# Kernel optimization log

Measured on AMD Instinct MI355X. Metric: run time of the kernel, lower is better.

Reference implementation:

```python
import jax, jax.numpy as jnp
import numpy as np
import math

# ---- hyperparameters taken verbatim from the source losses ----
NSAMPLE_REP = 20      # ballquery nsample in get_repulsion_loss
RADIUS_REP = 0.07     # ballquery radius in get_repulsion_loss
H_REP = 0.03          # kernel bandwidth h
PERCENTAGES = (0.004, 0.008, 0.01, 0.012, 0.016)
UNI_RADIUS = 1.0


def _gather(p, idx):
    # p: [B, N, 3], idx: [B, ...] int -> [B, ..., 3]  (pointops.grouping/gathering)
    return jax.vmap(lambda pts, i: pts[i])(p, idx)


def _ballquery(radius, nsample, q, p):
    # pointops.ballquery: for each query, first `nsample` point indices within
    # radius, padded with the first found index. q:[B,M,3], p:[B,N,3] -> [B,M,nsample]
    d = jnp.sum((q[:, :, None, :] - p[:, None, :, :]) ** 2, -1)  # [B,M,N]
    N = p.shape[1]
    keys = jnp.where(d <= radius * radius,
                     jnp.arange(N, dtype=jnp.int32)[None, None, :], N)
    idx = jnp.sort(keys, axis=-1)[..., :nsample]
    return jnp.where(idx >= N, idx[..., :1], idx)  # pad misses with first hit


def _fps(pcd, npoint):
    # pointops.furthestsampling on [B,N,3] -> [B,npoint] int32
    B, N, _ = pcd.shape
    bidx = jnp.arange(B)

    def step(carry, _):
        dist, far = carry                         # [B,N], [B]
        pt = pcd[bidx, far]                       # [B,3]
        d = jnp.sum((pcd - pt[:, None, :]) ** 2, -1)
        dist = jnp.minimum(dist, d)
        nxt = jnp.argmax(dist, -1).astype(jnp.int32)
        return (dist, nxt), far

    init = (jnp.full((B, N), 1e10, pcd.dtype), jnp.zeros((B,), jnp.int32))
    _, idxs = jax.lax.scan(step, init, None, length=npoint)
    return idxs.T  # [B, npoint]


def _repulsion_loss(pred):
    # pred: [B, N, 3]
    idx = _ballquery(RADIUS_REP, NSAMPLE_REP, pred, pred)   # [B,N,20], detached ints
    g = _gather(pred, idx) - pred[:, :, None, :]            # [B,N,20,3]
    dists = jnp.sum(g * g, -1)                              # [B,N,20]
    vals, _ = jax.lax.top_k(-dists, 5)                      # 5 smallest sq-dists
    d5 = jnp.maximum(-vals[:, :, 1:], 0.0)                  # drop self, ReLU
    ds = jnp.sqrt(d5)
    w = jnp.exp(-d5 / (H_REP * H_REP))
    return jnp.mean(RADIUS_REP - ds * w)


def _uniform_loss(pcd):
    # pcd: [B, N, 3]
    N = pcd.shape[1]
    npoint = int(N * 0.05)
    # FPS is called with identical args for every percentage -> compute once.
    fps_idx = _fps(jax.lax.stop_gradient(pcd), npoint)
    new_xyz = _gather(pcd, fps_idx)                          # [B,npoint,3]
    loss = jnp.zeros((), pcd.dtype)
    for p in PERCENTAGES:
        nsample = int(N * p)
        r = math.sqrt(p * UNI_RADIUS)
        disk_area = math.pi * UNI_RADIUS ** 2 * p / nsample
        expect_len = math.sqrt(2 * disk_area / 1.732)
        idx = _ballquery(r, nsample, new_xyz, pcd)           # [B,npoint,nsample]
        grouped = _gather(pcd, idx).reshape(-1, nsample, 3)  # [B*npoint,nsample,3]
        # knn_point(2, grouped, grouped): pairwise sq-dists inside each disk
        d = jnp.sum((grouped[:, :, None, :] - grouped[:, None, :, :]) ** 2, -1)
        vals, _ = jax.lax.top_k(-d, 2)
        ud = -vals[:, :, 1:]                                  # nearest non-self sqdist
        ud = jnp.sqrt(jnp.abs(ud + 1e-8))
        ud = jnp.mean(ud, -1)
        ud = (ud - expect_len) ** 2 / (expect_len + 1e-8)
        loss = loss + jnp.mean(ud) * (p * 100.0) ** 2
    return loss / len(PERCENTAGES)


def setup_inputs() -> dict:
    key = jax.random.key(0)
    # refined upsampled cloud: B=4, r*N = 4*2048 = 8192 points in [-1,1]^3
    pcd = jax.random.uniform(key, (4, 8192, 3), jnp.float32) * 2.0 - 1.0
    return {"pcd": pcd}


def reference(pcd):
    return jnp.stack([_uniform_loss(pcd), _repulsion_loss(pcd)])
```

## Files before the change

### kernel.cpp

```cpp
#include <hip/hip_runtime.h>
#include <hip/hip_bf16.h>
#include <cmath>
#include <cfloat>

#define BATCH 4
#define NPTS 8192
#define NPOINT 409
#define NBALLS (BATCH * NPOINT)
#define REP_NS 20
#define REP_QB 64
#define REP_SEG 8
#define SEG_LEN (NPTS / REP_SEG)
#define REP_BLOCKS (BATCH * NPTS / REP_QB)

#define WCAP 160
#define HCAP (4 * WCAP)

#define WS_FPS_OFF 0
#define WS_REP_OFF 8192
#define WS_UNI_OFF 12288

typedef float v2f __attribute__((ext_vector_type(2)));

struct UniParams {
  float  thr[5];
  float  e[5];
  float  eden[5];
  int    ns[5];
};

template <int CTRL>
__device__ __forceinline__ unsigned long long dpp_max_u64(unsigned long long key) {
  const int lo = __builtin_amdgcn_update_dpp(
      0, (int)(unsigned)(key & 0xFFFFFFFFull), CTRL, 0xf, 0xf, true);
  const int hi = __builtin_amdgcn_update_dpp(
      0, (int)(unsigned)(key >> 32), CTRL, 0xf, 0xf, true);
  const unsigned long long ok =
      ((unsigned long long)(unsigned)hi << 32) | (unsigned)lo;
  return ok > key ? ok : key;
}

__device__ __forceinline__ void ins5(float v, float& t0, float& t1, float& t2,
                                     float& t3, float& t4) {
  if (v < t4) {
    t4 = v;
    if (t4 < t3) { float tmp = t3; t3 = t4; t4 = tmp; }
    if (t3 < t2) { float tmp = t2; t2 = t3; t3 = tmp; }
    if (t2 < t1) { float tmp = t1; t1 = t2; t2 = tmp; }
    if (t1 < t0) { float tmp = t0; t0 = t1; t1 = tmp; }
  }
}

__device__ __forceinline__ float rep_term(float d) {
  d = fmaxf(d, 0.0f);
  return 0.07f - sqrtf(d) * expf(-(d / 0.0009f));
}

__global__ __launch_bounds__(512, 2) void fpsrep_kernel(const float* __restrict__ pcd,
                                                        int* __restrict__ fps_idx,
                                                        double* __restrict__ rep_part,
                                                        float rep_thr) {
  const int tid = threadIdx.x;
  const int lane = tid & 63;
  const int w = tid >> 6;
  extern __shared__ float smem[];

  if (blockIdx.x < BATCH) {
    const int b = blockIdx.x;
    const float* P = pcd + b * NPTS * 3;
    float* X = smem;
    float* Y = smem + NPTS;
    float* Z = smem + 2 * NPTS;

    for (int i = tid; i < NPTS; i += 512) {
      X[i] = P[i * 3 + 0];
      Y[i] = P[i * 3 + 1];
      Z[i] = P[i * 3 + 2];
    }

    v2f px[8], py[8], pz[8], dist[8];
    const int base = tid * 16;
#pragma unroll
    for (int k = 0; k < 8; k++) {
      const int i0 = (base + 2 * k) * 3;
      const int i1 = (base + 2 * k + 1) * 3;
      px[k] = (v2f){P[i0 + 0], P[i1 + 0]};
      py[k] = (v2f){P[i0 + 1], P[i1 + 1]};
      pz[k] = (v2f){P[i0 + 2], P[i1 + 2]};
      dist[k] = (v2f){1e10f, 1e10f};
    }
#pragma unroll
    for (int k = 0; k < 8; k++) {
      asm volatile("" : "+v"(px[k]), "+v"(py[k]), "+v"(pz[k]));
    }

    __shared__ unsigned long long s_key[2][8];
    __syncthreads();

    int far = 0;
    float fx = X[0], fy = Y[0], fz = Z[0];
    for (int s = 0; s < NPOINT; s++) {
      if (tid == 0) fps_idx[b * NPOINT + s] = far;

      const v2f fxv = (v2f){fx, fx};
      const v2f fyv = (v2f){fy, fy};
      const v2f fzv = (v2f){fz, fz};
      float best = -1.0f;
      int kb = 0;
#pragma unroll
      for (int k = 0; k < 8; k++) {
#pragma clang fp contract(off)
        const v2f dx = px[k] - fxv;
        const v2f dy = py[k] - fyv;
        const v2f dz = pz[k] - fzv;
        const v2f d  = (dx * dx + dy * dy) + dz * dz;
        const float n0 = fminf(dist[k].x, d.x);
        const float n1 = fminf(dist[k].y, d.y);
        dist[k].x = n0;
        dist[k].y = n1;
        if (n0 > best) { best = n0; kb = 2 * k; }
        if (n1 > best) { best = n1; kb = 2 * k + 1; }
      }
      const int bidx = base + kb;
      unsigned long long key =
          ((unsigned long long)__float_as_uint(best) << 32) |
          (unsigned long long)(0xFFFFFFFFu - (unsigned)bidx);

      key = dpp_max_u64<0x111>(key);
      key = dpp_max_u64<0x112>(key);
      key = dpp_max_u64<0x114>(key);
      key = dpp_max_u64<0x118>(key);
      key = dpp_max_u64<0x142>(key);
      key = dpp_max_u64<0x143>(key);

      const int par = s & 1;
      if (lane == 63) s_key[par][w] = key;
      __syncthreads();
      unsigned long long kbk = s_key[par][0];
#pragma unroll
      for (int w2 = 1; w2 < 8; w2++) {
        const unsigned long long kk = s_key[par][w2];
        if (kk > kbk) kbk = kk;
      }
      far = (int)(0xFFFFFFFFu - (unsigned)(kbk & 0xFFFFFFFFull));
      fx = X[far];
      fy = Y[far];
      fz = Z[far];
    }
    return;
  }

  __shared__ float s_t5[REP_SEG][REP_QB][5];
  __shared__ float s_d0[REP_SEG][REP_QB];
  __shared__ int   s_cnt[REP_SEG][REP_QB];

  const int blk = blockIdx.x - BATCH;
  const int b = blk >> 7;
  const int q = ((blk & 127) << 6) + lane;
  const float* P = pcd + b * NPTS * 3;

  const float qx = P[q * 3 + 0], qy = P[q * 3 + 1], qz = P[q * 3 + 2];

  int cnt = 0;
  float d0 = 0.0f;
  float t0 = FLT_MAX, t1 = FLT_MAX, t2 = FLT_MAX, t3 = FLT_MAX, t4 = FLT_MAX;

  const int wu = __builtin_amdgcn_readfirstlane(w);
  const float* S = P + wu * SEG_LEN * 3;
#pragma unroll 4
  for (int i = 0; i < SEG_LEN; i++) {
    const float x = S[i * 3 + 0];
    const float y = S[i * 3 + 1];
    const float z = S[i * 3 + 2];
    const float dx = qx - x, dy = qy - y, dz = qz - z;
    const float d = dx * dx + dy * dy + dz * dz;
    if (d <= rep_thr && cnt < REP_NS) {
      if (cnt == 0) d0 = d;
      ins5(d, t0, t1, t2, t3, t4);
      cnt++;
    }
  }

  s_t5[w][lane][0] = t0; s_t5[w][lane][1] = t1; s_t5[w][lane][2] = t2;
  s_t5[w][lane][3] = t3; s_t5[w][lane][4] = t4;
  s_d0[w][lane] = d0;
  s_cnt[w][lane] = cnt;
  __syncthreads();

  if (w == 0) {
    int total = 0;
    float fd0 = 0.0f;
    int first_seen = 0;
    float m0 = FLT_MAX, m1 = FLT_MAX, m2 = FLT_MAX, m3 = FLT_MAX, m4 = FLT_MAX;
#pragma unroll
    for (int sg = 0; sg < REP_SEG; sg++) {
      const int c = s_cnt[sg][lane];
      if (c > 0 && !first_seen) { fd0 = s_d0[sg][lane]; first_seen = 1; }
      total += c;
#pragma unroll
      for (int j = 0; j < 5; j++) ins5(s_t5[sg][lane][j], m0, m1, m2, m3, m4);
    }

    if (total > REP_NS) {
      int c2 = 0;
      m0 = FLT_MAX; m1 = FLT_MAX; m2 = FLT_MAX; m3 = FLT_MAX; m4 = FLT_MAX;
      for (int i = 0; i < NPTS && c2 < REP_NS; i++) {
        const float dx = qx - P[i * 3 + 0];
        const float dy = qy - P[i * 3 + 1];
        const float dz = qz - P[i * 3 + 2];
        const float d = dx * dx + dy * dy + dz * dz;
        if (d <= rep_thr) { ins5(d, m0, m1, m2, m3, m4); c2++; }
      }
    } else {
      for (int c = total; c < REP_NS; c++) ins5(fd0, m0, m1, m2, m3, m4);
    }

    float sum = rep_term(m1) + rep_term(m2) + rep_term(m3) + rep_term(m4);
#pragma unroll
    for (int off = 32; off >= 1; off >>= 1) sum += __shfl_down(sum, off);
    if (lane == 0) rep_part[blk] = (double)sum;
  }
}

__global__ __launch_bounds__(256) void uni_kernel(const float* __restrict__ pcd,
                                                  const int* __restrict__ fps_idx,
                                                  double* __restrict__ uni_part,
                                                  UniParams up) {
  const int ball = blockIdx.x;
  const int b = ball / NPOINT;
  const int tid = threadIdx.x;
  const int lane = tid & 63, w = tid >> 6;
  const float* P = pcd + b * NPTS * 3;

  const int qidx = fps_idx[ball];
  const float qx = P[qidx * 3 + 0], qy = P[qidx * 3 + 1], qz = P[qidx * 3 + 2];

  __shared__ float wx[4][WCAP], wy[4][WCAP], wz[4][WCAP], wd[4][WCAP];
  __shared__ int   s_wcnt[4];
  __shared__ float FX[HCAP], FY[HCAP], FZ[HCAP], FD[HCAP];
  __shared__ float CX[5][131], CY[5][131], CZ[5][131];
  __shared__ double dpart[4];

  int wcnt = 0;
  const float* S = P + w * 2048 * 3;
  for (int it = 0; it < 32; it++) {
    const int j = it * 64 + lane;
    const float x = S[j * 3 + 0];
    const float y = S[j * 3 + 1];
    const float z = S[j * 3 + 2];
    const float dx = qx - x, dy = qy - y, dz = qz - z;
    const float d = dx * dx + dy * dy + dz * dz;
    const bool hit = (d <= up.thr[4]);
    const unsigned long long m = __ballot(hit);
    if (hit) {
      const int pos = wcnt + __popcll(m & ((1ull << lane) - 1ull));
      if (pos < WCAP) {
        wx[w][pos] = x; wy[w][pos] = y; wz[w][pos] = z; wd[w][pos] = d;
      }
    }
    wcnt += __popcll(m);
  }
  if (lane == 0) s_wcnt[w] = min(wcnt, WCAP);
  __syncthreads();

  int off = 0;
#pragma unroll
  for (int w2 = 0; w2 < 4; w2++) {
    if (w2 == w) break;
    off += s_wcnt[w2];
  }
  for (int i = lane; i < s_wcnt[w]; i += 64) {
    FX[off + i] = wx[w][i]; FY[off + i] = wy[w][i];
    FZ[off + i] = wz[w][i]; FD[off + i] = wd[w][i];
  }
  __syncthreads();
  const int c = s_wcnt[0] + s_wcnt[1] + s_wcnt[2] + s_wcnt[3];

  const double wj_tab[5] = {0.16 / (5.0 * 1636.0 * 32.0),
                            0.64 / (5.0 * 1636.0 * 65.0),
                            1.0  / (5.0 * 1636.0 * 81.0),
                            1.44 / (5.0 * 1636.0 * 98.0),
                            2.56 / (5.0 * 1636.0 * 131.0)};

  double local = 0.0;
  for (int jp = w; jp < 5; jp += ((w == 0) ? 4 : 8)) {
    const float thr = up.thr[jp];
    const int nsj = up.ns[jp];

    int cnt2 = 0;
    for (int bse = 0; bse < c; bse += 64) {
      const int e = bse + lane;
      const bool pred = (e < c) && (FD[e] <= thr);
      const unsigned long long m = __ballot(pred);
      if (pred) {
        const int pos = cnt2 + __popcll(m & ((1ull << lane) - 1ull));
        if (pos < nsj) {
          CX[jp][pos] = FX[e]; CY[jp][pos] = FY[e]; CZ[jp][pos] = FZ[e];
        }
      }
      cnt2 += __popcll(m);
    }
    const int cj = min(cnt2, nsj);
    const int pads = nsj - cj;
    const int istart = (pads > 0) ? 1 : 0;

    if (pads > 0 && lane == 0) {
      const float ud = sqrtf(fabsf(1e-8f));
      const float dd = ud - up.e[jp];
      const float tt = (dd * dd) / up.eden[jp];
      local += (double)tt * wj_tab[jp] * (double)(pads + 1);
    }

    for (int r = istart + lane; r < cj; r += 64) {
      const float xi = CX[jp][r], yi = CY[jp][r], zi = CZ[jp][r];
      float m2 = FLT_MAX;
      for (int e2 = 0; e2 < cj; e2++) {
        if (e2 == r) continue;
        const float dx = xi - CX[jp][e2];
        const float dy = yi - CY[jp][e2];
        const float dz = zi - CZ[jp][e2];
        const float d = dx * dx + dy * dy + dz * dz;
        if (d < m2) m2 = d;
      }
      const float ud = sqrtf(fabsf(m2 + 1e-8f));
      const float dd = ud - up.e[jp];
      const float tt = (dd * dd) / up.eden[jp];
      local += (double)tt * wj_tab[jp];
    }
  }

#pragma unroll
  for (int o = 32; o >= 1; o >>= 1) local += __shfl_down(local, o);
  if (lane == 0) dpart[w] = local;
  __syncthreads();
  if (tid == 0) {
    uni_part[ball] = dpart[0] + dpart[1] + dpart[2] + dpart[3];
  }
}

__global__ __launch_bounds__(256) void fin_kernel(const double* __restrict__ rep_part,
                                                  const double* __restrict__ uni_part,
                                                  float* __restrict__ out) {
  __shared__ double sd[256];
  const int t = threadIdx.x;
  double u = 0.0, r = 0.0;
  for (int i = t; i < NBALLS; i += 256) u += uni_part[i];
  for (int i = t; i < REP_BLOCKS; i += 256) r += rep_part[i];

  sd[t] = u; __syncthreads();
  for (int s = 128; s > 0; s >>= 1) { if (t < s) sd[t] += sd[t + s]; __syncthreads(); }
  const double usum = sd[0];
  __syncthreads();
  sd[t] = r; __syncthreads();
  for (int s = 128; s > 0; s >>= 1) { if (t < s) sd[t] += sd[t + s]; __syncthreads(); }

  if (t == 0) {
    out[0] = (float)usum;
    out[1] = (float)(sd[0] * (1.0 / 131072.0));
  }
}

extern "C" void kernel_launch(void* const* d_in, const int* in_sizes, int n_in,
                              void* d_out, int out_size, void* d_ws, size_t ws_size,
                              hipStream_t stream) {
  (void)in_sizes; (void)n_in; (void)out_size; (void)ws_size;
  const float* pcd = (const float*)d_in[0];
  float* out = (float*)d_out;
  int*    fps      = (int*)((char*)d_ws + WS_FPS_OFF);
  double* rep_part = (double*)((char*)d_ws + WS_REP_OFF);
  double* uni_part = (double*)((char*)d_ws + WS_UNI_OFF);

  const float rep_thr = (float)(0.07 * 0.07);

  UniParams up;
  const double ps[5] = {0.004, 0.008, 0.01, 0.012, 0.016};
  for (int j = 0; j < 5; j++) {
    const int ns = (int)(8192.0 * ps[j]);
    const double r = sqrt(ps[j]);
    up.thr[j] = (float)(r * r);
    const double disk = M_PI * ps[j] / (double)ns;
    const double el = sqrt(2.0 * disk / 1.732);
    up.e[j] = (float)el;
    up.eden[j] = (float)(el + 1e-8);
    up.ns[j] = ns;
  }

  static const int kDynLds = NPTS * 3 * (int)sizeof(float);
  (void)hipFuncSetAttribute((const void*)fpsrep_kernel,
                            hipFuncAttributeMaxDynamicSharedMemorySize, kDynLds);

  fpsrep_kernel<<<BATCH + REP_BLOCKS, 512, kDynLds, stream>>>(pcd, fps, rep_part,
                                                              rep_thr);
  uni_kernel<<<NBALLS, 256, 0, stream>>>(pcd, fps, uni_part, up);
  fin_kernel<<<1, 256, 0, stream>>>(rep_part, uni_part, out);
}
```

Measured before the change: 447.1 us.

## Fuse FPS, repulsion and uniform loss into persistent kernel with spin-wait overlap

Merges the repulsion and uniform-loss work into one persistent kernel alongside the FPS blocks. Worker blocks fetch tasks from an atomic counter, and uniform-loss tasks spin on FPS indices that are published with atomic stores. The goal is to hide the uniform-loss pass behind the serial FPS chain instead of running it after a kernel boundary. The cost is spin-waiting, large LDS per worker block that caps residency, and 512-thread blocks with 8 warps for the uni tasks, where 3 warps idle in the per-percentage stage.

```diff
diff --git a/kernel.cpp b/kernel.cpp
--- a/kernel.cpp
+++ b/kernel.cpp
@@ -8,17 +8,19 @@
 #define NPOINT 409
 #define NBALLS (BATCH * NPOINT)
 #define REP_NS 20
-#define REP_QB 64
 #define REP_SEG 8
 #define SEG_LEN (NPTS / REP_SEG)
-#define REP_BLOCKS (BATCH * NPTS / REP_QB)
-
-#define WCAP 160
-#define HCAP (4 * WCAP)
+#define REP_TASKS 512
+#define NTASKS (REP_TASKS + NBALLS)
+#define NWORKERS 252
+
+#define UW 96
+#define UH (8 * UW)
 
 #define WS_FPS_OFF 0
 #define WS_REP_OFF 8192
 #define WS_UNI_OFF 12288
+#define WS_CNT_OFF 25600
 
 typedef float v2f __attribute__((ext_vector_type(2)));
 
@@ -56,14 +58,27 @@
   return 0.07f - sqrtf(d) * expf(-(d / 0.0009f));
 }
 
-__global__ __launch_bounds__(512, 2) void fpsrep_kernel(const float* __restrict__ pcd,
-                                                        int* __restrict__ fps_idx,
-                                                        double* __restrict__ rep_part,
-                                                        float rep_thr) {
+__global__ __launch_bounds__(512, 2) void fused_kernel(const float* __restrict__ pcd,
+                                                       int* __restrict__ fps_idx,
+                                                       double* __restrict__ rep_part,
+                                                       double* __restrict__ uni_part,
+                                                       int* __restrict__ counter,
+                                                       UniParams up, float rep_thr) {
   const int tid = threadIdx.x;
   const int lane = tid & 63;
   const int w = tid >> 6;
   extern __shared__ float smem[];
+
+  __shared__ unsigned long long s_key[2][8];
+  __shared__ float s_t5[REP_SEG][64][5];
+  __shared__ float s_d0[REP_SEG][64];
+  __shared__ int   s_cnt[REP_SEG][64];
+  __shared__ float wx[8][UW], wy[8][UW], wz[8][UW], wd[8][UW];
+  __shared__ int   s_wcnt[8];
+  __shared__ float FX[UH], FY[UH], FZ[UH], FD[UH];
+  __shared__ float CX[5][131], CY[5][131], CZ[5][131];
+  __shared__ double dpart[8];
+  __shared__ int s_task, s_qidx;
 
   if (blockIdx.x < BATCH) {
     const int b = blockIdx.x;
@@ -94,13 +109,15 @@
       asm volatile("" : "+v"(px[k]), "+v"(py[k]), "+v"(pz[k]));
     }
 
-    __shared__ unsigned long long s_key[2][8];
     __syncthreads();
 
     int far = 0;
     float fx = X[0], fy = Y[0], fz = Z[0];
     for (int s = 0; s < NPOINT; s++) {
-      if (tid == 0) fps_idx[b * NPOINT + s] = far;
+      if (tid == 0) {
+        __hip_atomic_store(&fps_idx[b * NPOINT + s], far,
+                           __ATOMIC_RELAXED, __HIP_MEMORY_SCOPE_AGENT);
+      }
 
       const v2f fxv = (v2f){fx, fx};
       const v2f fyv = (v2f){fy, fy};
@@ -150,191 +167,200 @@
     return;
   }
 
-  __shared__ float s_t5[REP_SEG][REP_QB][5];
-  __shared__ float s_d0[REP_SEG][REP_QB];
-  __shared__ int   s_cnt[REP_SEG][REP_QB];
-
-  const int blk = blockIdx.x - BATCH;
-  const int b = blk >> 7;
-  const int q = ((blk & 127) << 6) + lane;
-  const float* P = pcd + b * NPTS * 3;
-
-  const float qx = P[q * 3 + 0], qy = P[q * 3 + 1], qz = P[q * 3 + 2];
-
-  int cnt = 0;
-  float d0 = 0.0f;
-  float t0 = FLT_MAX, t1 = FLT_MAX, t2 = FLT_MAX, t3 = FLT_MAX, t4 = FLT_MAX;
-
-  const int wu = __builtin_amdgcn_readfirstlane(w);
-  const float* S = P + wu * SEG_LEN * 3;
-#pragma unroll 4
-  for (int i = 0; i < SEG_LEN; i++) {
-    const float x = S[i * 3 + 0];
-    const float y = S[i * 3 + 1];
-    const float z = S[i * 3 + 2];
-    const float dx = qx - x, dy = qy - y, dz = qz - z;
-    const float d = dx * dx + dy * dy + dz * dz;
-    if (d <= rep_thr && cnt < REP_NS) {
-      if (cnt == 0) d0 = d;
-      ins5(d, t0, t1, t2, t3, t4);
-      cnt++;
-    }
-  }
-
-  s_t5[w][lane][0] = t0; s_t5[w][lane][1] = t1; s_t5[w][lane][2] = t2;
-  s_t5[w][lane][3] = t3; s_t5[w][lane][4] = t4;
-  s_d0[w][lane] = d0;
-  s_cnt[w][lane] = cnt;
-  __syncthreads();
-
-  if (w == 0) {
-    int total = 0;
-    float fd0 = 0.0f;
-    int first_seen = 0;
-    float m0 = FLT_MAX, m1 = FLT_MAX, m2 = FLT_MAX, m3 = FLT_MAX, m4 = FLT_MAX;
-#pragma unroll
-    for (int sg = 0; sg < REP_SEG; sg++) {
-      const int c = s_cnt[sg][lane];
-      if (c > 0 && !first_seen) { fd0 = s_d0[sg][lane]; first_seen = 1; }
-      total += c;
-#pragma unroll
-      for (int j = 0; j < 5; j++) ins5(s_t5[sg][lane][j], m0, m1, m2, m3, m4);
-    }
-
-    if (total > REP_NS) {
-      int c2 = 0;
-      m0 = FLT_MAX; m1 = FLT_MAX; m2 = FLT_MAX; m3 = FLT_MAX; m4 = FLT_MAX;
-      for (int i = 0; i < NPTS && c2 < REP_NS; i++) {
-        const float dx = qx - P[i * 3 + 0];
-        const float dy = qy - P[i * 3 + 1];
-        const float dz = qz - P[i * 3 + 2];
-        const float d = dx * dx + dy * dy + dz * dz;
-        if (d <= rep_thr) { ins5(d, m0, m1, m2, m3, m4); c2++; }
-      }
-    } else {
-      for (int c = total; c < REP_NS; c++) ins5(fd0, m0, m1, m2, m3, m4);
-    }
-
-    float sum = rep_term(m1) + rep_term(m2) + rep_term(m3) + rep_term(m4);
-#pragma unroll
-    for (int off = 32; off >= 1; off >>= 1) sum += __shfl_down(sum, off);
-    if (lane == 0) rep_part[blk] = (double)sum;
-  }
-}
-
-__global__ __launch_bounds__(256) void uni_kernel(const float* __restrict__ pcd,
-                                                  const int* __restrict__ fps_idx,
-                                                  double* __restrict__ uni_part,
-                                                  UniParams up) {
-  const int ball = blockIdx.x;
-  const int b = ball / NPOINT;
-  const int tid = threadIdx.x;
-  const int lane = tid & 63, w = tid >> 6;
-  const float* P = pcd + b * NPTS * 3;
-
-  const int qidx = fps_idx[ball];
-  const float qx = P[qidx * 3 + 0], qy = P[qidx * 3 + 1], qz = P[qidx * 3 + 2];
-
-  __shared__ float wx[4][WCAP], wy[4][WCAP], wz[4][WCAP], wd[4][WCAP];
-  __shared__ int   s_wcnt[4];
-  __shared__ float FX[HCAP], FY[HCAP], FZ[HCAP], FD[HCAP];
-  __shared__ float CX[5][131], CY[5][131], CZ[5][131];
-  __shared__ double dpart[4];
-
-  int wcnt = 0;
-  const float* S = P + w * 2048 * 3;
-  for (int it = 0; it < 32; it++) {
-    const int j = it * 64 + lane;
-    const float x = S[j * 3 + 0];
-    const float y = S[j * 3 + 1];
-    const float z = S[j * 3 + 2];
-    const float dx = qx - x, dy = qy - y, dz = qz - z;
-    const float d = dx * dx + dy * dy + dz * dz;
-    const bool hit = (d <= up.thr[4]);
-    const unsigned long long m = __ballot(hit);
-    if (hit) {
-      const int pos = wcnt + __popcll(m & ((1ull << lane) - 1ull));
-      if (pos < WCAP) {
-        wx[w][pos] = x; wy[w][pos] = y; wz[w][pos] = z; wd[w][pos] = d;
-      }
-    }
-    wcnt += __popcll(m);
-  }
-  if (lane == 0) s_wcnt[w] = min(wcnt, WCAP);
-  __syncthreads();
-
-  int off = 0;
-#pragma unroll
-  for (int w2 = 0; w2 < 4; w2++) {
-    if (w2 == w) break;
-    off += s_wcnt[w2];
-  }
-  for (int i = lane; i < s_wcnt[w]; i += 64) {
-    FX[off + i] = wx[w][i]; FY[off + i] = wy[w][i];
-    FZ[off + i] = wz[w][i]; FD[off + i] = wd[w][i];
-  }
-  __syncthreads();
-  const int c = s_wcnt[0] + s_wcnt[1] + s_wcnt[2] + s_wcnt[3];
-
   const double wj_tab[5] = {0.16 / (5.0 * 1636.0 * 32.0),
                             0.64 / (5.0 * 1636.0 * 65.0),
                             1.0  / (5.0 * 1636.0 * 81.0),
                             1.44 / (5.0 * 1636.0 * 98.0),
                             2.56 / (5.0 * 1636.0 * 131.0)};
 
-  double local = 0.0;
-  for (int jp = w; jp < 5; jp += ((w == 0) ? 4 : 8)) {
-    const float thr = up.thr[jp];
-    const int nsj = up.ns[jp];
-
-    int cnt2 = 0;
-    for (int bse = 0; bse < c; bse += 64) {
-      const int e = bse + lane;
-      const bool pred = (e < c) && (FD[e] <= thr);
-      const unsigned long long m = __ballot(pred);
-      if (pred) {
-        const int pos = cnt2 + __popcll(m & ((1ull << lane) - 1ull));
-        if (pos < nsj) {
-          CX[jp][pos] = FX[e]; CY[jp][pos] = FY[e]; CZ[jp][pos] = FZ[e];
-        }
-      }
-      cnt2 += __popcll(m);
+  while (true) {
+    __syncthreads();
+    if (tid == 0) s_task = atomicAdd(counter, 1);
+    __syncthreads();
+    const int t = s_task;
+    if (t >= NTASKS) return;
+
+    if (t < REP_TASKS) {
+      const int b = t >> 7;
+      const int q = ((t & 127) << 6) + lane;
+      const float* P = pcd + b * NPTS * 3;
+
+      const float qx = P[q * 3 + 0], qy = P[q * 3 + 1], qz = P[q * 3 + 2];
+
+      int cnt = 0;
+      float d0 = 0.0f;
+      float t0 = FLT_MAX, t1 = FLT_MAX, t2 = FLT_MAX, t3 = FLT_MAX, t4 = FLT_MAX;
+
+      const int wu = __builtin_amdgcn_readfirstlane(w);
+      const float* S = P + wu * SEG_LEN * 3;
+#pragma unroll 4
+      for (int i = 0; i < SEG_LEN; i++) {
+        const float x = S[i * 3 + 0];
+        const float y = S[i * 3 + 1];
+        const float z = S[i * 3 + 2];
+        const float dx = qx - x, dy = qy - y, dz = qz - z;
+        const float d = dx * dx + dy * dy + dz * dz;
+        if (d <= rep_thr && cnt < REP_NS) {
+          if (cnt == 0) d0 = d;
+          ins5(d, t0, t1, t2, t3, t4);
+          cnt++;
+        }
+      }
+
+      s_t5[w][lane][0] = t0; s_t5[w][lane][1] = t1; s_t5[w][lane][2] = t2;
+      s_t5[w][lane][3] = t3; s_t5[w][lane][4] = t4;
+      s_d0[w][lane] = d0;
+      s_cnt[w][lane] = cnt;
+      __syncthreads();
+
+      if (w == 0) {
+        int total = 0;
+        float fd0 = 0.0f;
+        int first_seen = 0;
+        float m0 = FLT_MAX, m1 = FLT_MAX, m2 = FLT_MAX, m3 = FLT_MAX, m4 = FLT_MAX;
+#pragma unroll
+        for (int sg = 0; sg < REP_SEG; sg++) {
+          const int c = s_cnt[sg][lane];
+          if (c > 0 && !first_seen) { fd0 = s_d0[sg][lane]; first_seen = 1; }
+          total += c;
+#pragma unroll
+          for (int j = 0; j < 5; j++) ins5(s_t5[sg][lane][j], m0, m1, m2, m3, m4);
+        }
+
+        if (total > REP_NS) {
+          int c2 = 0;
+          m0 = FLT_MAX; m1 = FLT_MAX; m2 = FLT_MAX; m3 = FLT_MAX; m4 = FLT_MAX;
+          for (int i = 0; i < NPTS && c2 < REP_NS; i++) {
+            const float dx = qx - P[i * 3 + 0];
+            const float dy = qy - P[i * 3 + 1];
+            const float dz = qz - P[i * 3 + 2];
+            const float d = dx * dx + dy * dy + dz * dz;
+            if (d <= rep_thr) { ins5(d, m0, m1, m2, m3, m4); c2++; }
+          }
+        } else {
+          for (int c = total; c < REP_NS; c++) ins5(fd0, m0, m1, m2, m3, m4);
+        }
+
+        float sum = rep_term(m1) + rep_term(m2) + rep_term(m3) + rep_term(m4);
+#pragma unroll
+        for (int off = 32; off >= 1; off >>= 1) sum += __shfl_down(sum, off);
+        if (lane == 0) rep_part[t] = (double)sum;
+      }
+    } else {
+      const int ball = t - REP_TASKS;
+      const int b = ball / NPOINT;
+      const float* P = pcd + b * NPTS * 3;
+
+      if (tid == 0) {
+        int v = __hip_atomic_load(&fps_idx[ball], __ATOMIC_RELAXED,
+                                  __HIP_MEMORY_SCOPE_AGENT);
+        while (v < 0) {
+          __builtin_amdgcn_s_sleep(32);
+          v = __hip_atomic_load(&fps_idx[ball], __ATOMIC_RELAXED,
+                                __HIP_MEMORY_SCOPE_AGENT);
+        }
+        s_qidx = v;
+      }
+      __syncthreads();
+      const int qidx = s_qidx;
+      const float qx = P[qidx * 3 + 0], qy = P[qidx * 3 + 1], qz = P[qidx * 3 + 2];
+
+      int wcnt = 0;
+      const float* S = P + w * 1024 * 3;
+      for (int it = 0; it < 16; it++) {
+        const int j = it * 64 + lane;
+        const float x = S[j * 3 + 0];
+        const float y = S[j * 3 + 1];
+        const float z = S[j * 3 + 2];
+        const float dx = qx - x, dy = qy - y, dz = qz - z;
+        const float d = dx * dx + dy * dy + dz * dz;
+        const bool hit = (d <= up.thr[4]);
+        const unsigned long long m = __ballot(hit);
+        if (hit) {
+          const int pos = wcnt + __popcll(m & ((1ull << lane) - 1ull));
+          if (pos < UW) {
+            wx[w][pos] = x; wy[w][pos] = y; wz[w][pos] = z; wd[w][pos] = d;
+          }
+        }
+        wcnt += __popcll(m);
+      }
+      if (lane == 0) s_wcnt[w] = min(wcnt, UW);
+      __syncthreads();
+
+      int off = 0;
+#pragma unroll
+      for (int w2 = 0; w2 < 8; w2++) {
+        if (w2 == w) break;
+        off += s_wcnt[w2];
+      }
+      for (int i = lane; i < s_wcnt[w]; i += 64) {
+        FX[off + i] = wx[w][i]; FY[off + i] = wy[w][i];
+        FZ[off + i] = wz[w][i]; FD[off + i] = wd[w][i];
+      }
+      __syncthreads();
+      int c = 0;
+#pragma unroll
+      for (int w2 = 0; w2 < 8; w2++) c += s_wcnt[w2];
+
+      double local = 0.0;
+      if (w < 5) {
+        const int jp = w;
+        const float thr = up.thr[jp];
+        const int nsj = up.ns[jp];
+
+        int cnt2 = 0;
+        for (int bse = 0; bse < c; bse += 64) {
+          const int e = bse + lane;
+          const bool pred = (e < c) && (FD[e] <= thr);
+          const unsigned long long m = __ballot(pred);
+          if (pred) {
+            const int pos = cnt2 + __popcll(m & ((1ull << lane) - 1ull));
+            if (pos < nsj) {
+              CX[jp][pos] = FX[e]; CY[jp][pos] = FY[e]; CZ[jp][pos] = FZ[e];
+            }
+          }
+          cnt2 += __popcll(m);
+        }
+        const int cj = min(cnt2, nsj);
+        const int pads = nsj - cj;
+        const int istart = (pads > 0) ? 1 : 0;
+
+        if (pads > 0 && lane == 0) {
+          const float ud = sqrtf(fabsf(1e-8f));
+          const float dd = ud - up.e[jp];
+          const float tt = (dd * dd) / up.eden[jp];
+          local += (double)tt * wj_tab[jp] * (double)(pads + 1);
+        }
+
+        for (int r = istart + lane; r < cj; r += 64) {
+          const float xi = CX[jp][r], yi = CY[jp][r], zi = CZ[jp][r];
+          float m2 = FLT_MAX;
+          for (int e2 = 0; e2 < cj; e2++) {
+            if (e2 == r) continue;
+            const float dx = xi - CX[jp][e2];
+            const float dy = yi - CY[jp][e2];
+            const float dz = zi - CZ[jp][e2];
+            const float d = dx * dx + dy * dy + dz * dz;
+            if (d < m2) m2 = d;
+          }
+          const float ud = sqrtf(fabsf(m2 + 1e-8f));
+          const float dd = ud - up.e[jp];
+          const float tt = (dd * dd) / up.eden[jp];
+          local += (double)tt * wj_tab[jp];
+        }
+      }
+
+#pragma unroll
+      for (int o = 32; o >= 1; o >>= 1) local += __shfl_down(local, o);
+      if (lane == 0) dpart[w] = local;
+      __syncthreads();
+      if (tid == 0) {
+        double u = 0.0;
+#pragma unroll
+        for (int w2 = 0; w2 < 8; w2++) u += dpart[w2];
+        uni_part[ball] = u;
+      }
     }
-    const int cj = min(cnt2, nsj);
-    const int pads = nsj - cj;
-    const int istart = (pads > 0) ? 1 : 0;
-
-    if (pads > 0 && lane == 0) {
-      const float ud = sqrtf(fabsf(1e-8f));
-      const float dd = ud - up.e[jp];
-      const float tt = (dd * dd) / up.eden[jp];
-      local += (double)tt * wj_tab[jp] * (double)(pads + 1);
-    }
-
-    for (int r = istart + lane; r < cj; r += 64) {
-      const float xi = CX[jp][r], yi = CY[jp][r], zi = CZ[jp][r];
-      float m2 = FLT_MAX;
-      for (int e2 = 0; e2 < cj; e2++) {
-        if (e2 == r) continue;
-        const float dx = xi - CX[jp][e2];
-        const float dy = yi - CY[jp][e2];
-        const float dz = zi - CZ[jp][e2];
-        const float d = dx * dx + dy * dy + dz * dz;
-        if (d < m2) m2 = d;
-      }
-      const float ud = sqrtf(fabsf(m2 + 1e-8f));
-      const float dd = ud - up.e[jp];
-      const float tt = (dd * dd) / up.eden[jp];
-      local += (double)tt * wj_tab[jp];
-    }
-  }
-
-#pragma unroll
-  for (int o = 32; o >= 1; o >>= 1) local += __shfl_down(local, o);
-  if (lane == 0) dpart[w] = local;
-  __syncthreads();
-  if (tid == 0) {
-    uni_part[ball] = dpart[0] + dpart[1] + dpart[2] + dpart[3];
   }
 }
 
@@ -345,7 +371,7 @@
   const int t = threadIdx.x;
   double u = 0.0, r = 0.0;
   for (int i = t; i < NBALLS; i += 256) u += uni_part[i];
-  for (int i = t; i < REP_BLOCKS; i += 256) r += rep_part[i];
+  for (int i = t; i < REP_TASKS; i += 256) r += rep_part[i];
 
   sd[t] = u; __syncthreads();
   for (int s = 128; s > 0; s >>= 1) { if (t < s) sd[t] += sd[t + s]; __syncthreads(); }
@@ -369,6 +395,7 @@
   int*    fps      = (int*)((char*)d_ws + WS_FPS_OFF);
   double* rep_part = (double*)((char*)d_ws + WS_REP_OFF);
   double* uni_part = (double*)((char*)d_ws + WS_UNI_OFF);
+  int*    counter  = (int*)((char*)d_ws + WS_CNT_OFF);
 
   const float rep_thr = (float)(0.07 * 0.07);
 
@@ -385,12 +412,15 @@
     up.ns[j] = ns;
   }
 
+  hipMemsetAsync(fps, 0xFF, NBALLS * sizeof(int), stream);
+  hipMemsetAsync(counter, 0, sizeof(int), stream);
+
   static const int kDynLds = NPTS * 3 * (int)sizeof(float);
-  (void)hipFuncSetAttribute((const void*)fpsrep_kernel,
+  (void)hipFuncSetAttribute((const void*)fused_kernel,
                             hipFuncAttributeMaxDynamicSharedMemorySize, kDynLds);
 
-  fpsrep_kernel<<<BATCH + REP_BLOCKS, 512, kDynLds, stream>>>(pcd, fps, rep_part,
-                                                              rep_thr);
-  uni_kernel<<<NBALLS, 256, 0, stream>>>(pcd, fps, uni_part, up);
+  fused_kernel<<<BATCH + NWORKERS, 512, kDynLds, stream>>>(pcd, fps, rep_part,
+                                                           uni_part, counter,
+                                                           up, rep_thr);
   fin_kernel<<<1, 256, 0, stream>>>(rep_part, uni_part, out);
 }
```

Result: faster. 434.0 us (-2.9%).
